# Performance work log

Measured on AMD Instinct MI355X. Metric: run time of the kernel, lower is better.

## Reference

```python
import jax, jax.numpy as jnp
import numpy as np

B, S, H = 2, 2048, 4096
NH, NKV, D = 32, 8, 128  # heads, kv heads, head_dim


def rotate_half(x):
    x1, x2 = jnp.split(x, 2, axis=-1)
    return jnp.concatenate((-x2, x1), axis=-1)


def setup_inputs() -> dict:
    key = jax.random.key(0)
    ks = jax.random.split(key, 5)
    hidden_states = jax.random.normal(ks[0], (B, S, H), jnp.float32) * 0.02
    wq = jax.random.normal(ks[1], (H, NH * D), jnp.float32) * 0.02
    wk = jax.random.normal(ks[2], (H, NKV * D), jnp.float32) * 0.02
    wv = jax.random.normal(ks[3], (H, NKV * D), jnp.float32) * 0.02
    wo = jax.random.normal(ks[4], (NH * D, H), jnp.float32) * 0.02
    # Llama rotary cache: emb = cat(freqs, freqs); cos/sin shape [S, D]
    inv_freq = 1.0 / (10000.0 ** (jnp.arange(0, D, 2, dtype=jnp.float32) / D))
    t = jnp.arange(S, dtype=jnp.float32)
    freqs = jnp.einsum('i,j->ij', t, inv_freq)
    emb = jnp.concatenate((freqs, freqs), axis=-1)
    cos, sin = jnp.cos(emb), jnp.sin(emb)
    # additive causal mask [S, S]
    causal = jnp.tril(jnp.ones((S, S), dtype=bool))
    attn_mask = jnp.where(causal, 0.0, -1e9).astype(jnp.float32)
    return {'hidden_states': hidden_states, 'wq': wq, 'wk': wk, 'wv': wv,
            'wo': wo, 'cos': cos, 'sin': sin, 'attn_mask': attn_mask}


def reference(hidden_states, wq, wk, wv, wo, cos, sin, attn_mask):
    b, s, _ = hidden_states.shape
    q = (hidden_states @ wq).reshape(b, s, NH, D)   # [b,s,nh,d]
    k = (hidden_states @ wk).reshape(b, s, NKV, D)  # [b,s,nkv,d]
    v = (hidden_states @ wv).reshape(b, s, NKV, D)
    c = cos[None, :, None, :]  # [1,s,1,d]
    sn = sin[None, :, None, :]
    q = q * c + rotate_half(q) * sn
    k = k * c + rotate_half(k) * sn
    # GQA: repeat KV heads to match query heads
    grp = NH // NKV
    k = jnp.repeat(k, grp, axis=2)
    v = jnp.repeat(v, grp, axis=2)
    scale = 1.0 / np.sqrt(D).astype(np.float32)
    scores = jnp.einsum('bqhd,bkhd->bhqk', q, k) * scale
    scores = scores + attn_mask[None, None, :, :]
    probs = jax.nn.softmax(scores, axis=-1)
    out = jnp.einsum('bhqk,bkhd->bqhd', probs, v).reshape(b, s, NH * D)
    return out @ wo
```

## Files before the change

### kernel.cpp

```cpp
#include <hip/hip_runtime.h>

typedef __attribute__((ext_vector_type(8))) short short8;
typedef __attribute__((ext_vector_type(4))) float f32x4;
typedef __attribute__((ext_vector_type(4))) int int4v;

__device__ __forceinline__ float bf2f(unsigned short u) {
  unsigned int x = ((unsigned int)u) << 16;
  float f;
  __builtin_memcpy(&f, &x, 4);
  return f;
}
__device__ __forceinline__ unsigned short f2bf(float f) {
  unsigned int x;
  __builtin_memcpy(&x, &f, 4);
  unsigned int r = (x + 0x7FFFu + ((x >> 16) & 1u)) >> 16;
  return (unsigned short)r;
}
__device__ __forceinline__ unsigned int cvtpk_bf16(float lo, float hi) {
  unsigned int r;
  asm("v_cvt_pk_bf16_f32 %0, %1, %2" : "=v"(r) : "v"(lo), "v"(hi));
  return r;
}
__device__ __forceinline__ int4v s8_to_i4(short8 v) {
  int4v r;
  __builtin_memcpy(&r, &v, 16);
  return r;
}
__device__ __forceinline__ short8 i4_to_s8(int4v v) {
  short8 r;
  __builtin_memcpy(&r, &v, 16);
  return r;
}
__device__ __forceinline__ short8 ld8_f32(const float* p) {
  f32x4 x = *(const f32x4*)p;
  f32x4 y = *(const f32x4*)(p + 4);
  short8 r;
  r[0] = (short)f2bf(x[0]); r[1] = (short)f2bf(x[1]);
  r[2] = (short)f2bf(x[2]); r[3] = (short)f2bf(x[3]);
  r[4] = (short)f2bf(y[0]); r[5] = (short)f2bf(y[1]);
  r[6] = (short)f2bf(y[2]); r[7] = (short)f2bf(y[3]);
  return r;
}

__device__ __forceinline__ void async16(unsigned short* lds, const unsigned short* g) {
  __builtin_amdgcn_global_load_lds(
      (const __attribute__((address_space(1))) void*)g,
      (__attribute__((address_space(3))) void*)lds, 16, 0, 0);
}

__global__ void downcast_f2b(const float* __restrict__ in,
                             unsigned short* __restrict__ out, int n8) {
  int i = blockIdx.x * 256 + threadIdx.x;
  if (i >= n8) return;
  *(short8*)(out + (size_t)i * 8) = ld8_f32(in + (size_t)i * 8);
}

__global__ void transpose_f2b(const float* __restrict__ in,
                              unsigned short* __restrict__ out, int R, int Ccols) {
  __shared__ unsigned short tile[32][33];
  const int c0 = blockIdx.x * 32;
  const int r0 = blockIdx.y * 32;
  const int tx = threadIdx.x, ty = threadIdx.y;
#pragma unroll
  for (int i = 0; i < 32; i += 8)
    tile[ty + i][tx] = f2bf(in[(size_t)(r0 + ty + i) * Ccols + (c0 + tx)]);
  __syncthreads();
#pragma unroll
  for (int i = 0; i < 32; i += 8)
    out[(size_t)(c0 + ty + i) * R + (r0 + tx)] = tile[tx][ty + i];
}

#define MFMA16(AF, B0, B1, N0, N1)                                                   \
  _Pragma("unroll") for (int mi = 0; mi < 8; mi++) {                                 \
    acc[mi][N0] = __builtin_amdgcn_mfma_f32_16x16x32_bf16(AF[mi], B0, acc[mi][N0], 0, 0, 0); \
    acc[mi][N1] = __builtin_amdgcn_mfma_f32_16x16x32_bf16(AF[mi], B1, acc[mi][N1], 0, 0, 0); \
  }

#define STAGE8(BUF, SLOT, BASE, KOFF)                                     \
  do {                                                                    \
    async16(&lds[BUF][SLOT][tid * 8], (BASE) + (KOFF));                   \
    async16(&lds[BUF][SLOT][4096 + tid * 8], (BASE) + Kstep128 + (KOFF)); \
  } while (0)

#define BAR8 asm volatile("s_barrier" ::: "memory")

#define TILE8(CUR, UU, S0, S123, VM)                                                   \
  do {                                                                                 \
    const int kb = (UU)*64;                                                            \
    short8 af[8], b0, b1;                                                              \
                                                                       \
    _Pragma("unroll") for (int mi = 0; mi < 8; mi++)                                   \
        af[mi] = *(const short8*)(&lds[CUR][0][(wr * 128 + mi * 16 + fr) * 32 + fragoff]); \
    b0 = *(const short8*)(&lds[CUR][2][(wc * 64 + 0 * 16 + fr) * 32 + fragoff]);       \
    b1 = *(const short8*)(&lds[CUR][2][(wc * 64 + 1 * 16 + fr) * 32 + fragoff]);       \
    if (S0) STAGE8((CUR) ^ 1, 3, Bbase, kb + 96);                                      \
    BAR8;                                                                              \
    __builtin_amdgcn_s_setprio(1);                                                     \
    MFMA16(af, b0, b1, 0, 1);                                                          \
    __builtin_amdgcn_s_setprio(0);                                                     \
    BAR8;                                                                              \
                                                                       \
    b0 = *(const short8*)(&lds[CUR][2][(wc * 64 + 2 * 16 + fr) * 32 + fragoff]);       \
    b1 = *(const short8*)(&lds[CUR][2][(wc * 64 + 3 * 16 + fr) * 32 + fragoff]);       \
    if (S123) STAGE8(CUR, 0, Abase, kb + 128);                                         \
    BAR8;                                                                              \
    __builtin_amdgcn_s_setprio(1);                                                     \
    MFMA16(af, b0, b1, 2, 3);                                                          \
    __builtin_amdgcn_s_setprio(0);                                                     \
    BAR8;                                                                              \
                                                                       \
    _Pragma("unroll") for (int mi = 0; mi < 8; mi++)                                   \
        af[mi] = *(const short8*)(&lds[CUR][1][(wr * 128 + mi * 16 + fr) * 32 + fragoff]); \
    b0 = *(const short8*)(&lds[CUR][3][(wc * 64 + 0 * 16 + fr) * 32 + fragoff]);       \
    b1 = *(const short8*)(&lds[CUR][3][(wc * 64 + 1 * 16 + fr) * 32 + fragoff]);       \
    if (S123) STAGE8(CUR, 2, Bbase, kb + 128);                                         \
    BAR8;                                                                              \
    __builtin_amdgcn_s_setprio(1);                                                     \
    MFMA16(af, b0, b1, 0, 1);                                                          \
    __builtin_amdgcn_s_setprio(0);                                                     \
    BAR8;                                                                              \
                                                                       \
    b0 = *(const short8*)(&lds[CUR][3][(wc * 64 + 2 * 16 + fr) * 32 + fragoff]);       \
    b1 = *(const short8*)(&lds[CUR][3][(wc * 64 + 3 * 16 + fr) * 32 + fragoff]);       \
    if (S123) STAGE8(CUR, 1, Abase, kb + 160);                                         \
    BAR8;                                                                              \
    __builtin_amdgcn_s_setprio(1);                                                     \
    MFMA16(af, b0, b1, 2, 3);                                                          \
    __builtin_amdgcn_s_setprio(0);                                                     \
    if ((VM) == 6) {                                                                   \
      asm volatile("s_waitcnt vmcnt(6)" ::: "memory");                                 \
      __builtin_amdgcn_sched_barrier(0);                                               \
    } else if ((VM) == 0) {                                                            \
      asm volatile("s_waitcnt vmcnt(0)" ::: "memory");                                 \
      __builtin_amdgcn_sched_barrier(0);                                               \
    }                                                                                  \
    BAR8;                                                                              \
  } while (0)

template <int CF32>
__global__ __launch_bounds__(512, 2) void gemm8p(
    const unsigned short* __restrict__ A, const unsigned short* __restrict__ BT,
    void* __restrict__ Cp, int M, int N, int K) {
  alignas(16) __shared__ unsigned short lds[2][4][8192];
  const int tid = threadIdx.x;
  const int l = tid & 63;
  const int wv = tid >> 6;
  const int wr = wv >> 2, wc = wv & 3;

  const int nwg = gridDim.x * gridDim.y;
  int id = blockIdx.y * gridDim.x + blockIdx.x;
  id = (id & 7) * (nwg >> 3) + (id >> 3);
  const int bm = (id % gridDim.x) * 256;
  const int bn = (id / gridDim.x) * 256;

  const int fr = l & 15, hi = l >> 4;
  const int fragoff = ((hi ^ (((fr >> 3) & 1) << 1)) << 3);
  const int srow = tid >> 2;
  const int scol = (((tid & 3) ^ (((tid >> 5) & 1) << 1)) << 3);
  const unsigned short* Abase = A + (size_t)(bm + srow) * K + scol;
  const unsigned short* Bbase = BT + (size_t)(bn + srow) * K + scol;
  const size_t Kstep128 = (size_t)128 * K;

  f32x4 acc[8][4] = {};
  const int nt = K >> 6;

  STAGE8(0, 0, Abase, 0);
  STAGE8(0, 2, Bbase, 0);
  STAGE8(0, 1, Abase, 32);
  STAGE8(0, 3, Bbase, 32);
  STAGE8(1, 0, Abase, 64);
  STAGE8(1, 2, Bbase, 64);
  STAGE8(1, 1, Abase, 96);
  asm volatile("s_waitcnt vmcnt(6)" ::: "memory");
  __builtin_amdgcn_sched_barrier(0);
  BAR8;

  int U = 0;
  for (; U + 3 < nt; U += 2) {
    TILE8(0, U, 1, 1, 6);
    TILE8(1, U + 1, 1, 1, 6);
  }
  TILE8(0, nt - 2, 1, 0, 0);
  TILE8(1, nt - 1, 0, 0, -1);

  const int er = hi << 2;
#pragma unroll
  for (int mi = 0; mi < 8; mi++) {
#pragma unroll
    for (int ni = 0; ni < 4; ni++) {
      int row = bm + wr * 128 + mi * 16 + er;
      int col = bn + wc * 64 + ni * 16 + fr;
#pragma unroll
      for (int r = 0; r < 4; r++) {
        if constexpr (CF32)
          ((float*)Cp)[(size_t)(row + r) * N + col] = acc[mi][ni][r];
        else
          ((unsigned short*)Cp)[(size_t)(row + r) * N + col] = f2bf(acc[mi][ni][r]);
      }
    }
  }
}

__global__ void rope_kernel(unsigned short* __restrict__ buf,
                            const float* __restrict__ cosb,
                            const float* __restrict__ sinb,
                            int nh_shift, int rstride, int total) {
  int gid = blockIdx.x * 256 + threadIdx.x;
  if (gid >= total) return;
  int dblk = gid & 7;
  int u = gid >> 3;
  int head = u & ((1 << nh_shift) - 1);
  int token = u >> nh_shift;
  int s = token & 2047;
  int d0 = dblk << 3;
  unsigned short* p0 = buf + (size_t)token * rstride + (head << 7) + d0;
  unsigned short* p1 = p0 + 64;
  const float* cp = cosb + s * 128 + d0;
  const float* sp = sinb + s * 128 + d0;
  short8 a = *(const short8*)p0;
  short8 bq = *(const short8*)p1;
  f32x4 c0 = *(const f32x4*)cp, c1 = *(const f32x4*)(cp + 4);
  f32x4 s0 = *(const f32x4*)sp, s1 = *(const f32x4*)(sp + 4);
  short8 o0, o1;
#pragma unroll
  for (int j = 0; j < 8; j++) {
    float x0 = bf2f((unsigned short)a[j]);
    float x1 = bf2f((unsigned short)bq[j]);
    float c = (j < 4) ? c0[j & 3] : c1[j & 3];
    float sn = (j < 4) ? s0[j & 3] : s1[j & 3];
    o0[j] = (short)f2bf(x0 * c - x1 * sn);
    o1[j] = (short)f2bf(x1 * c + x0 * sn);
  }
  *(short8*)p0 = o0;
  *(short8*)p1 = o1;
}

#define ATT_SCALE 0.08838834764831845f
#define NEGBIG -30000.0f

__device__ __forceinline__ int vswz(int d) { return (((d >> 3) ^ d) & 7) << 2; }

__global__ __launch_bounds__(256, 2) void flash_attn(
    const unsigned short* __restrict__ Q, const unsigned short* __restrict__ KV,
    unsigned short* __restrict__ O) {
  alignas(16) __shared__ unsigned short lK[64 * 128];
  alignas(16) __shared__ unsigned int lV[128 * 32];

  const int tid = threadIdx.x;
  const int lane = tid & 63;
  const int w = tid >> 6;
  const int b = blockIdx.z;
  const int h = blockIdx.y;
  const int xa = blockIdx.x;
  const int kvh = h >> 2;

  const int fr = lane & 15;
  const int hi = lane >> 4;
  const int fk8 = hi << 3;
  const int hi4 = hi << 2;

  const int srow = tid >> 4;
  const int sc8 = (tid & 15) << 3;
  const int parity = srow & 1;

  const unsigned short* Kbp = KV + (size_t)(b * 2048) * 2048 + kvh * 128;
  const unsigned short* Vbp = Kbp + 1024;

  for (int pass = 0; pass < 2; pass++) {
    const int x = pass ? (15 - xa) : xa;
    const int q0 = x * 128;
    const int nt = 2 * x + 2;

    short8 qf[2][4];
#pragma unroll
    for (int qsub = 0; qsub < 2; qsub++) {
      const unsigned short* qb =
          Q + (size_t)(b * 2048 + q0 + w * 32 + qsub * 16 + fr) * 4096 + h * 128 + fk8;
#pragma unroll
      for (int ks = 0; ks < 4; ks++) qf[qsub][ks] = *(const short8*)(qb + ks * 32);
    }

    f32x4 oacc[2][8] = {};
    float m2[2] = {NEGBIG, NEGBIG};
    float ls[2] = {0.f, 0.f};

    short8 kreg[4], vreg[4];
#pragma unroll
    for (int rep = 0; rep < 4; rep++) {
      kreg[rep] = *(const short8*)(Kbp + (size_t)(rep * 16 + srow) * 2048 + sc8);
      vreg[rep] = *(const short8*)(Vbp + (size_t)(rep * 16 + srow) * 2048 + sc8);
    }

    for (int t = 0; t < nt; t++) {
      __syncthreads();
#pragma unroll
      for (int rep = 0; rep < 4; rep++)
        *(short8*)(lK + (rep * 16 + srow) * 128 + (sc8 ^ ((srow & 7) << 3))) = kreg[rep];
#pragma unroll
      for (int rep = 0; rep < 4; rep++) {
        int4v own = s8_to_i4(vreg[rep]);
        int4v oth;
#pragma unroll
        for (int q = 0; q < 4; q++) oth[q] = __shfl_xor(own[q], 16);
        unsigned int oA = parity ? (unsigned)own[2] : (unsigned)own[0];
        unsigned int oB = parity ? (unsigned)own[3] : (unsigned)own[1];
        unsigned int tA = parity ? (unsigned)oth[2] : (unsigned)oth[0];
        unsigned int tB = parity ? (unsigned)oth[3] : (unsigned)oth[1];
        unsigned int evA = parity ? tA : oA, odA = parity ? oA : tA;
        unsigned int evB = parity ? tB : oB, odB = parity ? oB : tB;
        int d0 = sc8 + (parity << 2);
        int kvp = rep * 8 + (srow >> 1);
        lV[(d0 + 0) * 32 + (kvp ^ vswz(d0 + 0))] = (evA & 0xFFFFu) | (odA << 16);
        lV[(d0 + 1) * 32 + (kvp ^ vswz(d0 + 1))] = (evA >> 16) | (odA & 0xFFFF0000u);
        lV[(d0 + 2) * 32 + (kvp ^ vswz(d0 + 2))] = (evB & 0xFFFFu) | (odB << 16);
        lV[(d0 + 3) * 32 + (kvp ^ vswz(d0 + 3))] = (evB >> 16) | (odB & 0xFFFF0000u);
      }
      __syncthreads();

      if (t + 1 < nt) {
        const int kv1 = (t + 1) * 64;
#pragma unroll
        for (int rep = 0; rep < 4; rep++) {
          kreg[rep] = *(const short8*)(Kbp + (size_t)(kv1 + rep * 16 + srow) * 2048 + sc8);
          vreg[rep] = *(const short8*)(Vbp + (size_t)(kv1 + rep * 16 + srow) * 2048 + sc8);
        }
      }

      f32x4 sacc[2][4] = {};
      __builtin_amdgcn_s_setprio(1);
#pragma unroll
      for (int fc = 0; fc < 4; fc++)
#pragma unroll
        for (int ks = 0; ks < 4; ks++) {
          short8 bk = *(const short8*)(lK + (fc * 16 + fr) * 128 +
                                       ((ks * 32 + fk8) ^ ((fr & 7) << 3)));
          sacc[0][fc] = __builtin_amdgcn_mfma_f32_16x16x32_bf16(bk, qf[0][ks], sacc[0][fc], 0, 0, 0);
          sacc[1][fc] = __builtin_amdgcn_mfma_f32_16x16x32_bf16(bk, qf[1][ks], sacc[1][fc], 0, 0, 0);
        }
      __builtin_amdgcn_s_setprio(0);

      const bool diag = (t >= nt - 2);
      const int kvb = t * 64;
      unsigned int pk[2][4][2];

#pragma unroll
      for (int qsub = 0; qsub < 2; qsub++) {
        const int q = q0 + w * 32 + qsub * 16 + fr;
        float sv[4][4];
#pragma unroll
        for (int fc = 0; fc < 4; fc++)
#pragma unroll
          for (int r = 0; r < 4; r++) {
            float xx = sacc[qsub][fc][r] * ATT_SCALE;
            if (diag && (kvb + fc * 16 + hi4 + r > q)) xx = NEGBIG;
            sv[fc][r] = xx;
          }
        float mx = sv[0][0];
#pragma unroll
        for (int fc = 0; fc < 4; fc++)
#pragma unroll
          for (int r = 0; r < 4; r++) mx = fmaxf(mx, sv[fc][r]);
        mx = fmaxf(mx, __shfl_xor(mx, 16));
        mx = fmaxf(mx, __shfl_xor(mx, 32));
        float mnew = fmaxf(m2[qsub], mx);
        float alpha = __expf(m2[qsub] - mnew);
        m2[qsub] = mnew;
        float rs = 0.f;
        float p[4][4];
#pragma unroll
        for (int fc = 0; fc < 4; fc++)
#pragma unroll
          for (int r = 0; r < 4; r++) {
            p[fc][r] = __expf(sv[fc][r] - mnew);
            rs += p[fc][r];
          }
        rs += __shfl_xor(rs, 16);
        rs += __shfl_xor(rs, 32);
        ls[qsub] = ls[qsub] * alpha + rs;
#pragma unroll
        for (int fc = 0; fc < 4; fc++) {
          pk[qsub][fc][0] = cvtpk_bf16(p[fc][0], p[fc][1]);
          pk[qsub][fc][1] = cvtpk_bf16(p[fc][2], p[fc][3]);
        }
        f32x4 av;
#pragma unroll
        for (int r = 0; r < 4; r++) av[r] = __shfl(alpha, hi4 + r);
#pragma unroll
        for (int nf = 0; nf < 8; nf++) oacc[qsub][nf] *= av;
      }

      const int src0 = fr + ((hi & 1) << 5);
      const int src1 = src0 + 16;
#pragma unroll
      for (int kvs = 0; kvs < 2; kvs++) {
        unsigned int aw[2][4];
#pragma unroll
        for (int qsub = 0; qsub < 2; qsub++) {
#pragma unroll
          for (int jj = 0; jj < 4; jj++) {
            int src = (jj < 2) ? src0 : src1;
            int rr = jj & 1;
            unsigned int y0 = (unsigned)__shfl((int)pk[qsub][kvs * 2][rr], src);
            unsigned int y1 = (unsigned)__shfl((int)pk[qsub][kvs * 2 + 1][rr], src);
            aw[qsub][jj] = (hi >> 1) ? y1 : y0;
          }
        }
        int4v a0i = {(int)aw[0][0], (int)aw[0][1], (int)aw[0][2], (int)aw[0][3]};
        int4v a1i = {(int)aw[1][0], (int)aw[1][1], (int)aw[1][2], (int)aw[1][3]};
        short8 af0 = i4_to_s8(a0i), af1 = i4_to_s8(a1i);
        __builtin_amdgcn_s_setprio(1);
#pragma unroll
        for (int nf = 0; nf < 8; nf++) {
          int row = nf * 16 + fr;
          int4v bvw = *(const int4v*)(lV + row * 32 + ((kvs * 16 + hi4) ^ vswz(row)));
          short8 bv = i4_to_s8(bvw);
          oacc[0][nf] = __builtin_amdgcn_mfma_f32_16x16x32_bf16(af0, bv, oacc[0][nf], 0, 0, 0);
          oacc[1][nf] = __builtin_amdgcn_mfma_f32_16x16x32_bf16(af1, bv, oacc[1][nf], 0, 0, 0);
        }
        __builtin_amdgcn_s_setprio(0);
      }
    }

#pragma unroll
    for (int qsub = 0; qsub < 2; qsub++) {
      f32x4 iv;
#pragma unroll
      for (int r = 0; r < 4; r++) iv[r] = 1.0f / __shfl(ls[qsub], hi4 + r);
#pragma unroll
      for (int r = 0; r < 4; r++) {
        unsigned short* op =
            O + (size_t)(b * 2048 + q0 + w * 32 + qsub * 16 + hi4 + r) * 4096 + h * 128 + fr;
#pragma unroll
        for (int nf = 0; nf < 8; nf++) op[nf * 16] = f2bf(oacc[qsub][nf][r] * iv[r]);
      }
    }
  }
}

extern "C" void kernel_launch(void* const* d_in, const int* in_sizes, int n_in,
                              void* d_out, int out_size, void* d_ws, size_t ws_size,
                              hipStream_t stream) {
  const float* hs = (const float*)d_in[0];
  const float* wq = (const float*)d_in[1];
  const float* wk = (const float*)d_in[2];
  const float* wv = (const float*)d_in[3];
  const float* wo = (const float*)d_in[4];
  const float* cosb = (const float*)d_in[5];
  const float* sinb = (const float*)d_in[6];

  unsigned short* ws = (unsigned short*)d_ws;
  unsigned short* T1 = ws;
  unsigned short* T2 = T1 + 16777216;
  unsigned short* T3 = T2 + 4194304;
  unsigned short* Qb = T3 + 4194304;
  unsigned short* KVb = Qb + 16777216;
  unsigned short* Ob = KVb + 8388608;

  unsigned short* hsb = (unsigned short*)d_out;

  dim3 tb(32, 8);
  downcast_f2b<<<8192, 256, 0, stream>>>(hs, hsb, 2097152);
  transpose_f2b<<<dim3(128, 128), tb, 0, stream>>>(wq, T1, 4096, 4096);
  transpose_f2b<<<dim3(32, 128), tb, 0, stream>>>(wk, T2, 4096, 1024);
  transpose_f2b<<<dim3(32, 128), tb, 0, stream>>>(wv, T3, 4096, 1024);

  gemm8p<0><<<dim3(16, 16), 512, 0, stream>>>(hsb, T1, Qb, 4096, 4096, 4096);
  gemm8p<0><<<dim3(16, 8), 512, 0, stream>>>(hsb, T2, KVb, 4096, 2048, 4096);

  transpose_f2b<<<dim3(128, 128), tb, 0, stream>>>(wo, T1, 4096, 4096);

  rope_kernel<<<4096, 256, 0, stream>>>(Qb, cosb, sinb, 5, 4096, 4096 * 32 * 8);
  rope_kernel<<<1024, 256, 0, stream>>>(KVb, cosb, sinb, 3, 2048, 4096 * 8 * 8);

  flash_attn<<<dim3(8, 32, 2), 256, 0, stream>>>(Qb, KVb, Ob);

  gemm8p<1><<<dim3(16, 16), 512, 0, stream>>>(Ob, T1, (float*)d_out, 4096, 4096, 4096);
}
```

Measured before the change: 548.5 us.

## Fold softmax scale into Q rope, use exp2 with lazy rescale, one tile per block

The softmax scale and log2(e) are folded into the Q RoPE kernel, so attention uses the hardware v_exp_f32 (exp2) directly instead of scaling each score and calling __expf. The running-max rescale of the output accumulators now happens only when some lane's new max exceeds the old one by more than 8, which skips most per-tile rescale multiplies. The two-pass causal load balancing (block x and 15-x) is replaced by one q-tile per block over a grid twice as large, with the heaviest tiles launched first. The deferred rescale lets exponents grow up to 2^8 before renormalising, which costs some precision headroom in bf16 P and fp32 accumulators.

```diff
diff --git a/kernel.cpp b/kernel.cpp
--- a/kernel.cpp
+++ b/kernel.cpp
@@ -19,6 +19,11 @@
 __device__ __forceinline__ unsigned int cvtpk_bf16(float lo, float hi) {
   unsigned int r;
   asm("v_cvt_pk_bf16_f32 %0, %1, %2" : "=v"(r) : "v"(lo), "v"(hi));
+  return r;
+}
+__device__ __forceinline__ float exp2_hw(float x) {
+  float r;
+  asm("v_exp_f32 %0, %1" : "=v"(r) : "v"(x));
   return r;
 }
 __device__ __forceinline__ int4v s8_to_i4(short8 v) {
@@ -204,7 +209,7 @@
 __global__ void rope_kernel(unsigned short* __restrict__ buf,
                             const float* __restrict__ cosb,
                             const float* __restrict__ sinb,
-                            int nh_shift, int rstride, int total) {
+                            int nh_shift, int rstride, int total, float oscale) {
   int gid = blockIdx.x * 256 + threadIdx.x;
   if (gid >= total) return;
   int dblk = gid & 7;
@@ -228,14 +233,13 @@
     float x1 = bf2f((unsigned short)bq[j]);
     float c = (j < 4) ? c0[j & 3] : c1[j & 3];
     float sn = (j < 4) ? s0[j & 3] : s1[j & 3];
-    o0[j] = (short)f2bf(x0 * c - x1 * sn);
-    o1[j] = (short)f2bf(x1 * c + x0 * sn);
+    o0[j] = (short)f2bf((x0 * c - x1 * sn) * oscale);
+    o1[j] = (short)f2bf((x1 * c + x0 * sn) * oscale);
   }
   *(short8*)p0 = o0;
   *(short8*)p1 = o1;
 }
 
-#define ATT_SCALE 0.08838834764831845f
 #define NEGBIG -30000.0f
 
 __device__ __forceinline__ int vswz(int d) { return (((d >> 3) ^ d) & 7) << 2; }
@@ -251,7 +255,7 @@
   const int w = tid >> 6;
   const int b = blockIdx.z;
   const int h = blockIdx.y;
-  const int xa = blockIdx.x;
+  const int x = 15 - blockIdx.x;
   const int kvh = h >> 2;
 
   const int fr = lane & 15;
@@ -266,173 +270,173 @@
   const unsigned short* Kbp = KV + (size_t)(b * 2048) * 2048 + kvh * 128;
   const unsigned short* Vbp = Kbp + 1024;
 
-  for (int pass = 0; pass < 2; pass++) {
-    const int x = pass ? (15 - xa) : xa;
-    const int q0 = x * 128;
-    const int nt = 2 * x + 2;
-
-    short8 qf[2][4];
+  const int q0 = x * 128;
+  const int nt = 2 * x + 2;
+
+  short8 qf[2][4];
+#pragma unroll
+  for (int qsub = 0; qsub < 2; qsub++) {
+    const unsigned short* qb =
+        Q + (size_t)(b * 2048 + q0 + w * 32 + qsub * 16 + fr) * 4096 + h * 128 + fk8;
+#pragma unroll
+    for (int ks = 0; ks < 4; ks++) qf[qsub][ks] = *(const short8*)(qb + ks * 32);
+  }
+
+  f32x4 oacc[2][8] = {};
+  float m2[2] = {NEGBIG, NEGBIG};
+  float ls[2] = {0.f, 0.f};
+
+  short8 kreg[4], vreg[4];
+#pragma unroll
+  for (int rep = 0; rep < 4; rep++) {
+    kreg[rep] = *(const short8*)(Kbp + (size_t)(rep * 16 + srow) * 2048 + sc8);
+    vreg[rep] = *(const short8*)(Vbp + (size_t)(rep * 16 + srow) * 2048 + sc8);
+  }
+
+  for (int t = 0; t < nt; t++) {
+    __syncthreads();
+#pragma unroll
+    for (int rep = 0; rep < 4; rep++)
+      *(short8*)(lK + (rep * 16 + srow) * 128 + (sc8 ^ ((srow & 7) << 3))) = kreg[rep];
+#pragma unroll
+    for (int rep = 0; rep < 4; rep++) {
+      int4v own = s8_to_i4(vreg[rep]);
+      int4v oth;
+#pragma unroll
+      for (int q = 0; q < 4; q++) oth[q] = __shfl_xor(own[q], 16);
+      unsigned int oA = parity ? (unsigned)own[2] : (unsigned)own[0];
+      unsigned int oB = parity ? (unsigned)own[3] : (unsigned)own[1];
+      unsigned int tA = parity ? (unsigned)oth[2] : (unsigned)oth[0];
+      unsigned int tB = parity ? (unsigned)oth[3] : (unsigned)oth[1];
+      unsigned int evA = parity ? tA : oA, odA = parity ? oA : tA;
+      unsigned int evB = parity ? tB : oB, odB = parity ? oB : tB;
+      int d0 = sc8 + (parity << 2);
+      int kvp = rep * 8 + (srow >> 1);
+      lV[(d0 + 0) * 32 + (kvp ^ vswz(d0 + 0))] = (evA & 0xFFFFu) | (odA << 16);
+      lV[(d0 + 1) * 32 + (kvp ^ vswz(d0 + 1))] = (evA >> 16) | (odA & 0xFFFF0000u);
+      lV[(d0 + 2) * 32 + (kvp ^ vswz(d0 + 2))] = (evB & 0xFFFFu) | (odB << 16);
+      lV[(d0 + 3) * 32 + (kvp ^ vswz(d0 + 3))] = (evB >> 16) | (odB & 0xFFFF0000u);
+    }
+    __syncthreads();
+
+    if (t + 1 < nt) {
+      const int kv1 = (t + 1) * 64;
+#pragma unroll
+      for (int rep = 0; rep < 4; rep++) {
+        kreg[rep] = *(const short8*)(Kbp + (size_t)(kv1 + rep * 16 + srow) * 2048 + sc8);
+        vreg[rep] = *(const short8*)(Vbp + (size_t)(kv1 + rep * 16 + srow) * 2048 + sc8);
+      }
+    }
+
+    f32x4 sacc[2][4] = {};
+    __builtin_amdgcn_s_setprio(1);
+#pragma unroll
+    for (int fc = 0; fc < 4; fc++)
+#pragma unroll
+      for (int ks = 0; ks < 4; ks++) {
+        short8 bk = *(const short8*)(lK + (fc * 16 + fr) * 128 +
+                                     ((ks * 32 + fk8) ^ ((fr & 7) << 3)));
+        sacc[0][fc] = __builtin_amdgcn_mfma_f32_16x16x32_bf16(bk, qf[0][ks], sacc[0][fc], 0, 0, 0);
+        sacc[1][fc] = __builtin_amdgcn_mfma_f32_16x16x32_bf16(bk, qf[1][ks], sacc[1][fc], 0, 0, 0);
+      }
+    __builtin_amdgcn_s_setprio(0);
+
+    const bool diag = (t >= nt - 2);
+    const int kvb = t * 64;
+    unsigned int pk[2][4][2];
+
 #pragma unroll
     for (int qsub = 0; qsub < 2; qsub++) {
-      const unsigned short* qb =
-          Q + (size_t)(b * 2048 + q0 + w * 32 + qsub * 16 + fr) * 4096 + h * 128 + fk8;
-#pragma unroll
-      for (int ks = 0; ks < 4; ks++) qf[qsub][ks] = *(const short8*)(qb + ks * 32);
-    }
-
-    f32x4 oacc[2][8] = {};
-    float m2[2] = {NEGBIG, NEGBIG};
-    float ls[2] = {0.f, 0.f};
-
-    short8 kreg[4], vreg[4];
-#pragma unroll
-    for (int rep = 0; rep < 4; rep++) {
-      kreg[rep] = *(const short8*)(Kbp + (size_t)(rep * 16 + srow) * 2048 + sc8);
-      vreg[rep] = *(const short8*)(Vbp + (size_t)(rep * 16 + srow) * 2048 + sc8);
-    }
-
-    for (int t = 0; t < nt; t++) {
-      __syncthreads();
-#pragma unroll
-      for (int rep = 0; rep < 4; rep++)
-        *(short8*)(lK + (rep * 16 + srow) * 128 + (sc8 ^ ((srow & 7) << 3))) = kreg[rep];
-#pragma unroll
-      for (int rep = 0; rep < 4; rep++) {
-        int4v own = s8_to_i4(vreg[rep]);
-        int4v oth;
-#pragma unroll
-        for (int q = 0; q < 4; q++) oth[q] = __shfl_xor(own[q], 16);
-        unsigned int oA = parity ? (unsigned)own[2] : (unsigned)own[0];
-        unsigned int oB = parity ? (unsigned)own[3] : (unsigned)own[1];
-        unsigned int tA = parity ? (unsigned)oth[2] : (unsigned)oth[0];
-        unsigned int tB = parity ? (unsigned)oth[3] : (unsigned)oth[1];
-        unsigned int evA = parity ? tA : oA, odA = parity ? oA : tA;
-        unsigned int evB = parity ? tB : oB, odB = parity ? oB : tB;
-        int d0 = sc8 + (parity << 2);
-        int kvp = rep * 8 + (srow >> 1);
-        lV[(d0 + 0) * 32 + (kvp ^ vswz(d0 + 0))] = (evA & 0xFFFFu) | (odA << 16);
-        lV[(d0 + 1) * 32 + (kvp ^ vswz(d0 + 1))] = (evA >> 16) | (odA & 0xFFFF0000u);
-        lV[(d0 + 2) * 32 + (kvp ^ vswz(d0 + 2))] = (evB & 0xFFFFu) | (odB << 16);
-        lV[(d0 + 3) * 32 + (kvp ^ vswz(d0 + 3))] = (evB >> 16) | (odB & 0xFFFF0000u);
-      }
-      __syncthreads();
-
-      if (t + 1 < nt) {
-        const int kv1 = (t + 1) * 64;
-#pragma unroll
-        for (int rep = 0; rep < 4; rep++) {
-          kreg[rep] = *(const short8*)(Kbp + (size_t)(kv1 + rep * 16 + srow) * 2048 + sc8);
-          vreg[rep] = *(const short8*)(Vbp + (size_t)(kv1 + rep * 16 + srow) * 2048 + sc8);
+      const int q = q0 + w * 32 + qsub * 16 + fr;
+      float sv[4][4];
+#pragma unroll
+      for (int fc = 0; fc < 4; fc++)
+#pragma unroll
+        for (int r = 0; r < 4; r++) {
+          float xx = sacc[qsub][fc][r];
+          if (diag && (kvb + fc * 16 + hi4 + r > q)) xx = NEGBIG;
+          sv[fc][r] = xx;
         }
-      }
-
-      f32x4 sacc[2][4] = {};
+      float mx = sv[0][0];
+#pragma unroll
+      for (int fc = 0; fc < 4; fc++)
+#pragma unroll
+        for (int r = 0; r < 4; r++) mx = fmaxf(mx, sv[fc][r]);
+      mx = fmaxf(mx, __shfl_xor(mx, 16));
+      mx = fmaxf(mx, __shfl_xor(mx, 32));
+      if (__any(mx > m2[qsub] + 8.0f)) {
+        float mnew = fmaxf(m2[qsub], mx);
+        float alpha = exp2_hw(m2[qsub] - mnew);
+        m2[qsub] = mnew;
+        ls[qsub] *= alpha;
+        f32x4 av;
+#pragma unroll
+        for (int r = 0; r < 4; r++) av[r] = __shfl(alpha, hi4 + r);
+#pragma unroll
+        for (int nf = 0; nf < 8; nf++) oacc[qsub][nf] *= av;
+      }
+      float rs = 0.f;
+      float p[4][4];
+#pragma unroll
+      for (int fc = 0; fc < 4; fc++)
+#pragma unroll
+        for (int r = 0; r < 4; r++) {
+          p[fc][r] = exp2_hw(sv[fc][r] - m2[qsub]);
+          rs += p[fc][r];
+        }
+      rs += __shfl_xor(rs, 16);
+      rs += __shfl_xor(rs, 32);
+      ls[qsub] += rs;
+#pragma unroll
+      for (int fc = 0; fc < 4; fc++) {
+        pk[qsub][fc][0] = cvtpk_bf16(p[fc][0], p[fc][1]);
+        pk[qsub][fc][1] = cvtpk_bf16(p[fc][2], p[fc][3]);
+      }
+    }
+
+    const int src0 = fr + ((hi & 1) << 5);
+    const int src1 = src0 + 16;
+#pragma unroll
+    for (int kvs = 0; kvs < 2; kvs++) {
+      unsigned int aw[2][4];
+#pragma unroll
+      for (int qsub = 0; qsub < 2; qsub++) {
+#pragma unroll
+        for (int jj = 0; jj < 4; jj++) {
+          int src = (jj < 2) ? src0 : src1;
+          int rr = jj & 1;
+          unsigned int y0 = (unsigned)__shfl((int)pk[qsub][kvs * 2][rr], src);
+          unsigned int y1 = (unsigned)__shfl((int)pk[qsub][kvs * 2 + 1][rr], src);
+          aw[qsub][jj] = (hi >> 1) ? y1 : y0;
+        }
+      }
+      int4v a0i = {(int)aw[0][0], (int)aw[0][1], (int)aw[0][2], (int)aw[0][3]};
+      int4v a1i = {(int)aw[1][0], (int)aw[1][1], (int)aw[1][2], (int)aw[1][3]};
+      short8 af0 = i4_to_s8(a0i), af1 = i4_to_s8(a1i);
       __builtin_amdgcn_s_setprio(1);
 #pragma unroll
-      for (int fc = 0; fc < 4; fc++)
-#pragma unroll
-        for (int ks = 0; ks < 4; ks++) {
-          short8 bk = *(const short8*)(lK + (fc * 16 + fr) * 128 +
-                                       ((ks * 32 + fk8) ^ ((fr & 7) << 3)));
-          sacc[0][fc] = __builtin_amdgcn_mfma_f32_16x16x32_bf16(bk, qf[0][ks], sacc[0][fc], 0, 0, 0);
-          sacc[1][fc] = __builtin_amdgcn_mfma_f32_16x16x32_bf16(bk, qf[1][ks], sacc[1][fc], 0, 0, 0);
-        }
+      for (int nf = 0; nf < 8; nf++) {
+        int row = nf * 16 + fr;
+        int4v bvw = *(const int4v*)(lV + row * 32 + ((kvs * 16 + hi4) ^ vswz(row)));
+        short8 bv = i4_to_s8(bvw);
+        oacc[0][nf] = __builtin_amdgcn_mfma_f32_16x16x32_bf16(af0, bv, oacc[0][nf], 0, 0, 0);
+        oacc[1][nf] = __builtin_amdgcn_mfma_f32_16x16x32_bf16(af1, bv, oacc[1][nf], 0, 0, 0);
+      }
       __builtin_amdgcn_s_setprio(0);
-
-      const bool diag = (t >= nt - 2);
-      const int kvb = t * 64;
-      unsigned int pk[2][4][2];
-
-#pragma unroll
-      for (int qsub = 0; qsub < 2; qsub++) {
-        const int q = q0 + w * 32 + qsub * 16 + fr;
-        float sv[4][4];
-#pragma unroll
-        for (int fc = 0; fc < 4; fc++)
-#pragma unroll
-          for (int r = 0; r < 4; r++) {
-            float xx = sacc[qsub][fc][r] * ATT_SCALE;
-            if (diag && (kvb + fc * 16 + hi4 + r > q)) xx = NEGBIG;
-            sv[fc][r] = xx;
-          }
-        float mx = sv[0][0];
-#pragma unroll
-        for (int fc = 0; fc < 4; fc++)
-#pragma unroll
-          for (int r = 0; r < 4; r++) mx = fmaxf(mx, sv[fc][r]);
-        mx = fmaxf(mx, __shfl_xor(mx, 16));
-        mx = fmaxf(mx, __shfl_xor(mx, 32));
-        float mnew = fmaxf(m2[qsub], mx);
-        float alpha = __expf(m2[qsub] - mnew);
-        m2[qsub] = mnew;
-        float rs = 0.f;
-        float p[4][4];
-#pragma unroll
-        for (int fc = 0; fc < 4; fc++)
-#pragma unroll
-          for (int r = 0; r < 4; r++) {
-            p[fc][r] = __expf(sv[fc][r] - mnew);
-            rs += p[fc][r];
-          }
-        rs += __shfl_xor(rs, 16);
-        rs += __shfl_xor(rs, 32);
-        ls[qsub] = ls[qsub] * alpha + rs;
-#pragma unroll
-        for (int fc = 0; fc < 4; fc++) {
-          pk[qsub][fc][0] = cvtpk_bf16(p[fc][0], p[fc][1]);
-          pk[qsub][fc][1] = cvtpk_bf16(p[fc][2], p[fc][3]);
-        }
-        f32x4 av;
-#pragma unroll
-        for (int r = 0; r < 4; r++) av[r] = __shfl(alpha, hi4 + r);
-#pragma unroll
-        for (int nf = 0; nf < 8; nf++) oacc[qsub][nf] *= av;
-      }
-
-      const int src0 = fr + ((hi & 1) << 5);
-      const int src1 = src0 + 16;
-#pragma unroll
-      for (int kvs = 0; kvs < 2; kvs++) {
-        unsigned int aw[2][4];
-#pragma unroll
-        for (int qsub = 0; qsub < 2; qsub++) {
-#pragma unroll
-          for (int jj = 0; jj < 4; jj++) {
-            int src = (jj < 2) ? src0 : src1;
-            int rr = jj & 1;
-            unsigned int y0 = (unsigned)__shfl((int)pk[qsub][kvs * 2][rr], src);
-            unsigned int y1 = (unsigned)__shfl((int)pk[qsub][kvs * 2 + 1][rr], src);
-            aw[qsub][jj] = (hi >> 1) ? y1 : y0;
-          }
-        }
-        int4v a0i = {(int)aw[0][0], (int)aw[0][1], (int)aw[0][2], (int)aw[0][3]};
-        int4v a1i = {(int)aw[1][0], (int)aw[1][1], (int)aw[1][2], (int)aw[1][3]};
-        short8 af0 = i4_to_s8(a0i), af1 = i4_to_s8(a1i);
-        __builtin_amdgcn_s_setprio(1);
-#pragma unroll
-        for (int nf = 0; nf < 8; nf++) {
-          int row = nf * 16 + fr;
-          int4v bvw = *(const int4v*)(lV + row * 32 + ((kvs * 16 + hi4) ^ vswz(row)));
-          short8 bv = i4_to_s8(bvw);
-          oacc[0][nf] = __builtin_amdgcn_mfma_f32_16x16x32_bf16(af0, bv, oacc[0][nf], 0, 0, 0);
-          oacc[1][nf] = __builtin_amdgcn_mfma_f32_16x16x32_bf16(af1, bv, oacc[1][nf], 0, 0, 0);
-        }
-        __builtin_amdgcn_s_setprio(0);
-      }
-    }
-
-#pragma unroll
-    for (int qsub = 0; qsub < 2; qsub++) {
-      f32x4 iv;
-#pragma unroll
-      for (int r = 0; r < 4; r++) iv[r] = 1.0f / __shfl(ls[qsub], hi4 + r);
-#pragma unroll
-      for (int r = 0; r < 4; r++) {
-        unsigned short* op =
-            O + (size_t)(b * 2048 + q0 + w * 32 + qsub * 16 + hi4 + r) * 4096 + h * 128 + fr;
-#pragma unroll
-        for (int nf = 0; nf < 8; nf++) op[nf * 16] = f2bf(oacc[qsub][nf][r] * iv[r]);
-      }
+    }
+  }
+
+#pragma unroll
+  for (int qsub = 0; qsub < 2; qsub++) {
+    f32x4 iv;
+#pragma unroll
+    for (int r = 0; r < 4; r++) iv[r] = 1.0f / __shfl(ls[qsub], hi4 + r);
+#pragma unroll
+    for (int r = 0; r < 4; r++) {
+      unsigned short* op =
+          O + (size_t)(b * 2048 + q0 + w * 32 + qsub * 16 + hi4 + r) * 4096 + h * 128 + fr;
+#pragma unroll
+      for (int nf = 0; nf < 8; nf++) op[nf * 16] = f2bf(oacc[qsub][nf][r] * iv[r]);
     }
   }
 }
@@ -469,10 +473,11 @@
 
   transpose_f2b<<<dim3(128, 128), tb, 0, stream>>>(wo, T1, 4096, 4096);
 
-  rope_kernel<<<4096, 256, 0, stream>>>(Qb, cosb, sinb, 5, 4096, 4096 * 32 * 8);
-  rope_kernel<<<1024, 256, 0, stream>>>(KVb, cosb, sinb, 3, 2048, 4096 * 8 * 8);
-
-  flash_attn<<<dim3(8, 32, 2), 256, 0, stream>>>(Qb, KVb, Ob);
+  const float qscale = 0.08838834764831845f * 1.4426950408889634f;
+  rope_kernel<<<4096, 256, 0, stream>>>(Qb, cosb, sinb, 5, 4096, 4096 * 32 * 8, qscale);
+  rope_kernel<<<1024, 256, 0, stream>>>(KVb, cosb, sinb, 3, 2048, 4096 * 8 * 8, 1.0f);
+
+  flash_attn<<<dim3(16, 32, 2), 256, 0, stream>>>(Qb, KVb, Ob);
 
   gemm8p<1><<<dim3(16, 16), 512, 0, stream>>>(Ob, T1, (float*)d_out, 4096, 4096, 4096);
 }
```

Measured after the change: 633.8 us. 1.16x slower.
